# Performance work log

Measured on AMD Instinct MI355X. Metric: run time of the kernel, lower is better.

Reference implementation:

```python
import jax, jax.numpy as jnp
import numpy as np

N_NODES = 50000
N_EDGES = 800000
IN_CH = 128
H_CH = 128


def setup_inputs() -> dict:
    key = jax.random.key(0)
    ks = jax.random.split(key, 8)
    q = jax.random.normal(ks[0], (N_NODES, IN_CH), dtype=jnp.float32)
    k = jax.random.normal(ks[1], (N_NODES, IN_CH), dtype=jnp.float32)
    v = jax.random.normal(ks[2], (N_NODES, IN_CH), dtype=jnp.float32)
    envelope = jax.random.uniform(ks[3], (N_EDGES,), dtype=jnp.float32)
    edge_index = jax.random.randint(ks[4], (2, N_EDGES), 0, N_NODES, dtype=jnp.int64)
    # torch nn.Linear weights are [out, in]; init ~ U(-1/sqrt(fan_in), 1/sqrt(fan_in))
    s = 1.0 / np.sqrt(IN_CH)
    W_l = jax.random.uniform(ks[5], (H_CH, IN_CH), jnp.float32, -s, s)
    W_r = jax.random.uniform(ks[6], (H_CH, IN_CH), jnp.float32, -s, s)
    sa = 1.0 / np.sqrt(H_CH)
    attn_w = jax.random.uniform(ks[7], (1, H_CH), jnp.float32, -sa, sa)
    return {"q": q, "k": k, "v": v, "envelope": envelope,
            "W_l": W_l, "W_r": W_r, "attn_w": attn_w, "edge_index": edge_index}


def reference(q, k, v, envelope, W_l, W_r, attn_w, edge_index):
    # k, v are accepted but unused, matching the original module.
    N = q.shape[0]
    src = edge_index[0]
    dst = edge_index[1]
    g_l = q @ W_l.T                       # [N, H]
    g_r = q @ W_r.T                       # [N, H]
    g_l_src = g_l[src]                    # [E, H] gather
    g_sum = g_l_src + g_r[dst]            # [E, H]
    e = (jax.nn.silu(g_sum) @ attn_w.T)[:, 0]   # [E]
    e = e + jnp.log(envelope + 1e-7)
    # scatter_softmax over dst groups (numerically stable segment softmax)
    seg_max = jax.ops.segment_max(e, dst, num_segments=N)   # [N]
    ex = jnp.exp(e - seg_max[dst])                           # [E]
    denom = jax.ops.segment_sum(ex, dst, num_segments=N)     # [N]
    attn = ex / denom[dst]                                   # [E]
    out = jax.ops.segment_sum(attn[:, None] * g_l_src, dst, num_segments=N)  # [N, H]
    return out
```

## Files before the change

kernel.cpp:

```cpp
#include <hip/hip_runtime.h>
#include <math.h>

#define N_NODES 50000
#define N_EDGES 800000
#define CH 128
#define CAP 48
#define SCAT_BLOCKS ((N_EDGES + 255) / 256)
#define GEMM_BLOCKS ((N_NODES + 127) / 128)

typedef __attribute__((ext_vector_type(8))) short short8;
typedef __attribute__((ext_vector_type(4))) float f32x4;
union FragU { uint4 u; short8 s; };

__device__ __forceinline__ unsigned pack_bf16(float a, float b) {
    unsigned ua = __float_as_uint(a);
    unsigned ub = __float_as_uint(b);
    ua += 0x7FFFu + ((ua >> 16) & 1u);
    ub += 0x7FFFu + ((ub >> 16) & 1u);
    return (ua >> 16) | (ub & 0xFFFF0000u);
}

__global__ __launch_bounds__(256) void prep_pack_kernel(
    const float* __restrict__ W_l, const float* __restrict__ W_r,
    uint4* __restrict__ Wf4, int* __restrict__ counts)
{
    int tid = blockIdx.x * 256 + threadIdx.x;
    if (tid < 2 * 8 * 4 * 64) {
        int lane  = tid & 63;
        int chunk = (tid >> 6) & 3;
        int tile  = (tid >> 8) & 7;
        int mat   = tid >> 11;
        const float* W = mat ? W_r : W_l;
        int n  = tile * 16 + (lane & 15);
        int k0 = chunk * 32 + (lane >> 4) * 8;
        const float* wp = W + n * CH + k0;
        float4 a = *(const float4*)wp;
        float4 b = *(const float4*)(wp + 4);
        uint4 p;
        p.x = pack_bf16(a.x, a.y);
        p.y = pack_bf16(a.z, a.w);
        p.z = pack_bf16(b.x, b.y);
        p.w = pack_bf16(b.z, b.w);
        Wf4[tid] = p;
    }
    for (int i = tid; i < N_NODES; i += 64 * 256) counts[i] = 0;
}

__global__ __launch_bounds__(256) void scatter_kernel(
    const int* __restrict__ src, const int* __restrict__ dst,
    const float* __restrict__ env,
    int* __restrict__ counts, unsigned* __restrict__ recs)
{
    int i = blockIdx.x * 256 + threadIdx.x;
    if (i < N_EDGES) {
        int d = dst[i];
        int rank = atomicAdd(&counts[d], 1);
        if (rank < CAP) {
            unsigned ev = __float_as_uint(env[i] + 1e-7f);
            ev += 0x7FFFu + ((ev >> 16) & 1u);
            recs[d * CAP + rank] = (unsigned)src[i] | (ev & 0xFFFF0000u);
        }
    }
}

__global__ __launch_bounds__(512) void gemm_kernel(
    const float* __restrict__ q, const uint4* __restrict__ Wf4,
    unsigned short* __restrict__ g_l16, float* __restrict__ g_r)
{
    __shared__ uint4 sW[4096];
    for (int i = threadIdx.x; i < 4096; i += 512) sW[i] = Wf4[i];

    const int wv   = threadIdx.x >> 6;
    const int lane = threadIdx.x & 63;
    const int m    = lane & 15;
    const int quad = lane >> 4;
    const int row0 = blockIdx.x * 128 + wv * 16;

    int arow = row0 + m;
    if (arow >= N_NODES) arow = N_NODES - 1;
    const float* qr = q + (size_t)arow * CH + quad * 8;

    FragU A[4];
    #pragma unroll
    for (int c = 0; c < 4; ++c) {
        float4 x = *(const float4*)(qr + c * 32);
        float4 y = *(const float4*)(qr + c * 32 + 4);
        A[c].u.x = pack_bf16(x.x, x.y);
        A[c].u.y = pack_bf16(x.z, x.w);
        A[c].u.z = pack_bf16(y.x, y.y);
        A[c].u.w = pack_bf16(y.z, y.w);
    }

    __syncthreads();

    for (int mat = 0; mat < 2; ++mat) {
        for (int tile = 0; tile < 8; ++tile) {
            f32x4 acc = {0.f, 0.f, 0.f, 0.f};
            const uint4* bp = sW + (size_t)(mat * 8 + tile) * 256;
            #pragma unroll
            for (int c = 0; c < 4; ++c) {
                FragU B; B.u = bp[c * 64 + lane];
                acc = __builtin_amdgcn_mfma_f32_16x16x32_bf16(A[c].s, B.s, acc, 0, 0, 0);
            }
            int col = tile * 16 + m;
            #pragma unroll
            for (int r = 0; r < 4; ++r) {
                int rowg = row0 + quad * 4 + r;
                if (rowg < N_NODES) {
                    if (mat == 0) {
                        unsigned u = __float_as_uint(acc[r]);
                        u += 0x7FFFu + ((u >> 16) & 1u);
                        g_l16[(size_t)rowg * CH + col] = (unsigned short)(u >> 16);
                    } else {
                        g_r[(size_t)rowg * CH + col] = acc[r];
                    }
                }
            }
        }
    }
}

__global__ __launch_bounds__(256) void node_attn_kernel(
    const uint4* __restrict__ g_lb4, const float* __restrict__ g_r,
    const float* __restrict__ attn_w,
    const unsigned* __restrict__ recs, const int* __restrict__ counts,
    float* __restrict__ out)
{
    int gid = blockIdx.x * blockDim.x + threadIdx.x;
    int wid = gid >> 6;
    if (wid >= N_NODES) return;
    const int lane = threadIdx.x & 63;
    const int q4 = lane >> 4;
    const int sl = lane & 15;

    int cnt = counts[wid];
    if (cnt > CAP) cnt = CAP;

    float gr[8], aw[8];
    {
        const float4* grp = (const float4*)(g_r + (size_t)wid * CH + sl * 8);
        float4 a = grp[0], b = grp[1];
        gr[0] = a.x; gr[1] = a.y; gr[2] = a.z; gr[3] = a.w;
        gr[4] = b.x; gr[5] = b.y; gr[6] = b.z; gr[7] = b.w;
        const float4* awp = (const float4*)(attn_w + sl * 8);
        float4 c = awp[0], d = awp[1];
        aw[0] = c.x; aw[1] = c.y; aw[2] = c.z; aw[3] = c.w;
        aw[4] = d.x; aw[5] = d.y; aw[6] = d.z; aw[7] = d.w;
    }

    float l = 0.0f;
    float acc[8] = {0.f, 0.f, 0.f, 0.f, 0.f, 0.f, 0.f, 0.f};

    if (cnt > 0) {
        const int clampi = cnt - 1;
        unsigned rcl = recs[wid * CAP + min(lane, clampi)];
        const int G = (cnt + 3) >> 2;

        #define REC_OF(jg, rv) { int e_ = (jg) * 4 + q4; if (e_ > clampi) e_ = clampi; \
                                 rv = __shfl(rcl, e_, 64); }

        unsigned r0, r1, r2, r3;
        uint4 gA, gB, gC, gD;
        REC_OF(0, r0); gA = g_lb4[(size_t)(r0 & 0xFFFFu) * (CH / 8) + sl];
        r1 = r0; r2 = r0; gB = gA; gC = gA;
        if (G > 1) { REC_OF(1, r1); gB = g_lb4[(size_t)(r1 & 0xFFFFu) * (CH / 8) + sl]; }
        if (G > 2) { REC_OF(2, r2); gC = g_lb4[(size_t)(r2 & 0xFFFFu) * (CH / 8) + sl]; }

        for (int j = 0; j < G; ++j) {
            r3 = r0; gD = gA;
            if (j + 3 < G) {
                REC_OF(j + 3, r3);
                gD = g_lb4[(size_t)(r3 & 0xFFFFu) * (CH / 8) + sl];
            }

            bool active = (j * 4 + q4) < cnt;
            float ev = __uint_as_float(r0 & 0xFFFF0000u);

            float gl[8];
            gl[0] = __uint_as_float(gA.x << 16);
            gl[1] = __uint_as_float(gA.x & 0xFFFF0000u);
            gl[2] = __uint_as_float(gA.y << 16);
            gl[3] = __uint_as_float(gA.y & 0xFFFF0000u);
            gl[4] = __uint_as_float(gA.z << 16);
            gl[5] = __uint_as_float(gA.z & 0xFFFF0000u);
            gl[6] = __uint_as_float(gA.w << 16);
            gl[7] = __uint_as_float(gA.w & 0xFFFF0000u);

            float p = 0.0f;
            #pragma unroll
            for (int c = 0; c < 8; ++c) {
                float h = gl[c] + gr[c];
                float sg = __builtin_amdgcn_rcpf(1.0f + __expf(-h));
                p = fmaf(h * aw[c], sg, p);
            }
            p += __shfl_xor(p, 1, 64);
            p += __shfl_xor(p, 2, 64);
            p += __shfl_xor(p, 4, 64);
            p += __shfl_xor(p, 8, 64);

            float w = __expf(p) * (active ? ev : 0.0f);
            l += w;
            #pragma unroll
            for (int c = 0; c < 8; ++c) acc[c] = fmaf(w, gl[c], acc[c]);

            r0 = r1; gA = gB; r1 = r2; gB = gC; r2 = r3; gC = gD;
        }
        #undef REC_OF
    }

    #pragma unroll
    for (int o = 16; o <= 32; o <<= 1) {
        l += __shfl_xor(l, o, 64);
        #pragma unroll
        for (int c = 0; c < 8; ++c) acc[c] += __shfl_xor(acc[c], o, 64);
    }

    if (q4 == 0) {
        float inv = (l > 0.0f) ? __builtin_amdgcn_rcpf(l) : 0.0f;
        float4 o0 = {acc[0] * inv, acc[1] * inv, acc[2] * inv, acc[3] * inv};
        float4 o1 = {acc[4] * inv, acc[5] * inv, acc[6] * inv, acc[7] * inv};
        float4* op = (float4*)(out + (size_t)wid * CH + sl * 8);
        op[0] = o0;
        op[1] = o1;
    }
}

extern "C" void kernel_launch(void* const* d_in, const int* in_sizes, int n_in,
                              void* d_out, int out_size, void* d_ws, size_t ws_size,
                              hipStream_t stream)
{
    const float* q      = (const float*)d_in[0];
    const float* env    = (const float*)d_in[3];
    const float* W_l    = (const float*)d_in[4];
    const float* W_r    = (const float*)d_in[5];
    const float* attn_w = (const float*)d_in[6];
    const int*   eidx   = (const int*)d_in[7];
    const int* src = eidx;
    const int* dst = eidx + N_EDGES;
    float* out = (float*)d_out;

    float* ws    = (float*)d_ws;
    unsigned* g_lb = (unsigned*)ws;
    float* g_r   = (float*)(g_lb + (size_t)N_NODES * (CH / 2));
    uint4* Wf4   = (uint4*)(g_r + (size_t)N_NODES * CH);
    unsigned* recs = (unsigned*)(Wf4 + 4096);
    int* counts  = (int*)(recs + (size_t)N_NODES * CAP);

    prep_pack_kernel<<<64, 256, 0, stream>>>(W_l, W_r, Wf4, counts);

    scatter_kernel<<<SCAT_BLOCKS, 256, 0, stream>>>(src, dst, env, counts, recs);

    gemm_kernel<<<GEMM_BLOCKS, 512, 0, stream>>>(
        q, Wf4, (unsigned short*)g_lb, g_r);

    int node_wave_blocks = (N_NODES * 64 + 255) / 256;
    node_attn_kernel<<<node_wave_blocks, 256, 0, stream>>>(
        (const uint4*)g_lb, g_r, attn_w, recs, counts, out);
}
```

Before: 224.9 us.

## Store g_l as fp32 pre-scaled by log2e and use packed exp2 math

```diff
diff --git a/kernel.cpp b/kernel.cpp
--- a/kernel.cpp
+++ b/kernel.cpp
@@ -7,10 +7,14 @@
 #define CAP 48
 #define SCAT_BLOCKS ((N_EDGES + 255) / 256)
 #define GEMM_BLOCKS ((N_NODES + 127) / 128)
+#define LOG2E 1.44269504088896f
+#define LN2   0.69314718055995f
 
 typedef __attribute__((ext_vector_type(8))) short short8;
 typedef __attribute__((ext_vector_type(4))) float f32x4;
+typedef __attribute__((ext_vector_type(2))) float f32x2;
 union FragU { uint4 u; short8 s; };
+struct GL { f32x4 a, b; };
 
 __device__ __forceinline__ unsigned pack_bf16(float a, float b) {
     unsigned ua = __float_as_uint(a);
@@ -65,7 +69,7 @@
 
 __global__ __launch_bounds__(512) void gemm_kernel(
     const float* __restrict__ q, const uint4* __restrict__ Wf4,
-    unsigned short* __restrict__ g_l16, float* __restrict__ g_r)
+    float* __restrict__ g_lf, float* __restrict__ g_r)
 {
     __shared__ uint4 sW[4096];
     for (int i = threadIdx.x; i < 4096; i += 512) sW[i] = Wf4[i];
@@ -94,6 +98,7 @@
     __syncthreads();
 
     for (int mat = 0; mat < 2; ++mat) {
+        float* gout = mat ? g_r : g_lf;
         for (int tile = 0; tile < 8; ++tile) {
             f32x4 acc = {0.f, 0.f, 0.f, 0.f};
             const uint4* bp = sW + (size_t)(mat * 8 + tile) * 256;
@@ -106,22 +111,15 @@
             #pragma unroll
             for (int r = 0; r < 4; ++r) {
                 int rowg = row0 + quad * 4 + r;
-                if (rowg < N_NODES) {
-                    if (mat == 0) {
-                        unsigned u = __float_as_uint(acc[r]);
-                        u += 0x7FFFu + ((u >> 16) & 1u);
-                        g_l16[(size_t)rowg * CH + col] = (unsigned short)(u >> 16);
-                    } else {
-                        g_r[(size_t)rowg * CH + col] = acc[r];
-                    }
-                }
+                if (rowg < N_NODES)
+                    gout[(size_t)rowg * CH + col] = acc[r] * LOG2E;
             }
         }
     }
 }
 
 __global__ __launch_bounds__(256) void node_attn_kernel(
-    const uint4* __restrict__ g_lb4, const float* __restrict__ g_r,
+    const f32x4* __restrict__ g_lf4, const float* __restrict__ g_r,
     const float* __restrict__ attn_w,
     const unsigned* __restrict__ recs, const int* __restrict__ counts,
     float* __restrict__ out)
@@ -136,20 +134,20 @@
     int cnt = counts[wid];
     if (cnt > CAP) cnt = CAP;
 
-    float gr[8], aw[8];
+    f32x2 gr2[4], aw2[4];
     {
-        const float4* grp = (const float4*)(g_r + (size_t)wid * CH + sl * 8);
-        float4 a = grp[0], b = grp[1];
-        gr[0] = a.x; gr[1] = a.y; gr[2] = a.z; gr[3] = a.w;
-        gr[4] = b.x; gr[5] = b.y; gr[6] = b.z; gr[7] = b.w;
-        const float4* awp = (const float4*)(attn_w + sl * 8);
-        float4 c = awp[0], d = awp[1];
-        aw[0] = c.x; aw[1] = c.y; aw[2] = c.z; aw[3] = c.w;
-        aw[4] = d.x; aw[5] = d.y; aw[6] = d.z; aw[7] = d.w;
+        const f32x4* grp = (const f32x4*)(g_r + (size_t)wid * CH + sl * 8);
+        f32x4 a = grp[0], b = grp[1];
+        gr2[0] = (f32x2){a.x, a.y}; gr2[1] = (f32x2){a.z, a.w};
+        gr2[2] = (f32x2){b.x, b.y}; gr2[3] = (f32x2){b.z, b.w};
+        const f32x4* awp = (const f32x4*)(attn_w + sl * 8);
+        f32x4 c = awp[0], d = awp[1];
+        aw2[0] = (f32x2){c.x, c.y}; aw2[1] = (f32x2){c.z, c.w};
+        aw2[2] = (f32x2){d.x, d.y}; aw2[3] = (f32x2){d.z, d.w};
     }
 
     float l = 0.0f;
-    float acc[8] = {0.f, 0.f, 0.f, 0.f, 0.f, 0.f, 0.f, 0.f};
+    f32x2 acc2[4] = {{0.f,0.f},{0.f,0.f},{0.f,0.f},{0.f,0.f}};
 
     if (cnt > 0) {
         const int clampi = cnt - 1;
@@ -158,67 +156,80 @@
 
         #define REC_OF(jg, rv) { int e_ = (jg) * 4 + q4; if (e_ > clampi) e_ = clampi; \
                                  rv = __shfl(rcl, e_, 64); }
+        #define GATHER(rv, gv) { const f32x4* p_ = g_lf4 + \
+                                 (size_t)((rv) & 0xFFFFu) * (CH / 4) + sl * 2; \
+                                 gv.a = p_[0]; gv.b = p_[1]; }
 
         unsigned r0, r1, r2, r3;
-        uint4 gA, gB, gC, gD;
-        REC_OF(0, r0); gA = g_lb4[(size_t)(r0 & 0xFFFFu) * (CH / 8) + sl];
-        r1 = r0; r2 = r0; gB = gA; gC = gA;
-        if (G > 1) { REC_OF(1, r1); gB = g_lb4[(size_t)(r1 & 0xFFFFu) * (CH / 8) + sl]; }
-        if (G > 2) { REC_OF(2, r2); gC = g_lb4[(size_t)(r2 & 0xFFFFu) * (CH / 8) + sl]; }
+        GL g0, g1, g2, g3;
+        REC_OF(0, r0); GATHER(r0, g0);
+        r1 = r0; r2 = r0; g1 = g0; g2 = g0;
+        if (G > 1) { REC_OF(1, r1); GATHER(r1, g1); }
+        if (G > 2) { REC_OF(2, r2); GATHER(r2, g2); }
 
         for (int j = 0; j < G; ++j) {
-            r3 = r0; gD = gA;
+            r3 = r0; g3 = g0;
             if (j + 3 < G) {
                 REC_OF(j + 3, r3);
-                gD = g_lb4[(size_t)(r3 & 0xFFFFu) * (CH / 8) + sl];
+                GATHER(r3, g3);
             }
 
             bool active = (j * 4 + q4) < cnt;
             float ev = __uint_as_float(r0 & 0xFFFF0000u);
 
-            float gl[8];
-            gl[0] = __uint_as_float(gA.x << 16);
-            gl[1] = __uint_as_float(gA.x & 0xFFFF0000u);
-            gl[2] = __uint_as_float(gA.y << 16);
-            gl[3] = __uint_as_float(gA.y & 0xFFFF0000u);
-            gl[4] = __uint_as_float(gA.z << 16);
-            gl[5] = __uint_as_float(gA.z & 0xFFFF0000u);
-            gl[6] = __uint_as_float(gA.w << 16);
-            gl[7] = __uint_as_float(gA.w & 0xFFFF0000u);
-
-            float p = 0.0f;
-            #pragma unroll
-            for (int c = 0; c < 8; ++c) {
-                float h = gl[c] + gr[c];
-                float sg = __builtin_amdgcn_rcpf(1.0f + __expf(-h));
-                p = fmaf(h * aw[c], sg, p);
-            }
+            f32x2 glv[4];
+            glv[0] = (f32x2){g0.a.x, g0.a.y};
+            glv[1] = (f32x2){g0.a.z, g0.a.w};
+            glv[2] = (f32x2){g0.b.x, g0.b.y};
+            glv[3] = (f32x2){g0.b.z, g0.b.w};
+
+            f32x2 pv = {0.f, 0.f};
+            #pragma unroll
+            for (int c = 0; c < 4; ++c) {
+                f32x2 h = glv[c] + gr2[c];
+                f32x2 en;
+                en.x = __builtin_amdgcn_exp2f(-h.x);
+                en.y = __builtin_amdgcn_exp2f(-h.y);
+                f32x2 d1 = en + 1.0f;
+                f32x2 sg;
+                sg.x = __builtin_amdgcn_rcpf(d1.x);
+                sg.y = __builtin_amdgcn_rcpf(d1.y);
+                f32x2 t = h * aw2[c];
+                pv = __builtin_elementwise_fma(t, sg, pv);
+            }
+            float p = pv.x + pv.y;
             p += __shfl_xor(p, 1, 64);
             p += __shfl_xor(p, 2, 64);
             p += __shfl_xor(p, 4, 64);
             p += __shfl_xor(p, 8, 64);
 
-            float w = __expf(p) * (active ? ev : 0.0f);
+            float w = __builtin_amdgcn_exp2f(p) * (active ? ev : 0.0f);
             l += w;
-            #pragma unroll
-            for (int c = 0; c < 8; ++c) acc[c] = fmaf(w, gl[c], acc[c]);
-
-            r0 = r1; gA = gB; r1 = r2; gB = gC; r2 = r3; gC = gD;
+            f32x2 ws = {w, w};
+            #pragma unroll
+            for (int c = 0; c < 4; ++c)
+                acc2[c] = __builtin_elementwise_fma(ws, glv[c], acc2[c]);
+
+            r0 = r1; g0 = g1; r1 = r2; g1 = g2; r2 = r3; g2 = g3;
         }
         #undef REC_OF
+        #undef GATHER
     }
 
     #pragma unroll
     for (int o = 16; o <= 32; o <<= 1) {
         l += __shfl_xor(l, o, 64);
         #pragma unroll
-        for (int c = 0; c < 8; ++c) acc[c] += __shfl_xor(acc[c], o, 64);
+        for (int c = 0; c < 4; ++c) {
+            acc2[c].x += __shfl_xor(acc2[c].x, o, 64);
+            acc2[c].y += __shfl_xor(acc2[c].y, o, 64);
+        }
     }
 
     if (q4 == 0) {
-        float inv = (l > 0.0f) ? __builtin_amdgcn_rcpf(l) : 0.0f;
-        float4 o0 = {acc[0] * inv, acc[1] * inv, acc[2] * inv, acc[3] * inv};
-        float4 o1 = {acc[4] * inv, acc[5] * inv, acc[6] * inv, acc[7] * inv};
+        float inv = (l > 0.0f) ? __builtin_amdgcn_rcpf(l) * LN2 : 0.0f;
+        float4 o0 = {acc2[0].x * inv, acc2[0].y * inv, acc2[1].x * inv, acc2[1].y * inv};
+        float4 o1 = {acc2[2].x * inv, acc2[2].y * inv, acc2[3].x * inv, acc2[3].y * inv};
         float4* op = (float4*)(out + (size_t)wid * CH + sl * 8);
         op[0] = o0;
         op[1] = o1;
@@ -240,8 +251,8 @@
     float* out = (float*)d_out;
 
     float* ws    = (float*)d_ws;
-    unsigned* g_lb = (unsigned*)ws;
-    float* g_r   = (float*)(g_lb + (size_t)N_NODES * (CH / 2));
+    float* g_lf  = ws;
+    float* g_r   = g_lf + (size_t)N_NODES * CH;
     uint4* Wf4   = (uint4*)(g_r + (size_t)N_NODES * CH);
     unsigned* recs = (unsigned*)(Wf4 + 4096);
     int* counts  = (int*)(recs + (size_t)N_NODES * CAP);
@@ -250,10 +261,9 @@
 
     scatter_kernel<<<SCAT_BLOCKS, 256, 0, stream>>>(src, dst, env, counts, recs);
 
-    gemm_kernel<<<GEMM_BLOCKS, 512, 0, stream>>>(
-        q, Wf4, (unsigned short*)g_lb, g_r);
+    gemm_kernel<<<GEMM_BLOCKS, 512, 0, stream>>>(q, Wf4, g_lf, g_r);
 
     int node_wave_blocks = (N_NODES * 64 + 255) / 256;
     node_attn_kernel<<<node_wave_blocks, 256, 0, stream>>>(
-        (const uint4*)g_lb, g_r, attn_w, recs, counts, out);
-}
+        (const f32x4*)g_lf, g_r, attn_w, recs, counts, out);
+}
```

Result: slower. 236.0 us (+5.0%).
